# Kernel tuning notes

Hardware: AMD Instinct MI355X
Metric: run time of the kernel (lower is better)

## Reference

```python
import jax, jax.numpy as jnp
import numpy as np

N, E, B = 20000, 320000, 64   # nodes, edges, graphs
H, L = 32, 3                  # hidden dim (dim_inner), message passes
HH = H * H
IDX = jnp.array([[0, 1, 2, 3, 4, 5],
                 [1, 6, 7, 8, 9, 10],
                 [2, 7, 11, 12, 13, 14],
                 [3, 8, 12, 15, 16, 17],
                 [4, 9, 13, 16, 18, 19],
                 [5, 10, 14, 17, 19, 20]])


def setup_inputs() -> dict:
    key = jax.random.key(0)
    ks = iter(jax.random.split(key, 40))
    def nrm(shape, s=0.1):
        return jax.random.normal(next(ks), shape, jnp.float32) * s
    inp = {}
    inp['node_attrs'] = jax.random.normal(next(ks), (N, 1), jnp.float32)
    inp['positions'] = jax.random.normal(next(ks), (N, 3), jnp.float32)
    inp['shifts'] = jax.random.normal(next(ks), (E, 3), jnp.float32) * 0.01
    inp['edge_attr'] = jax.random.uniform(next(ks), (E, 1), jnp.float32)
    inp['edge_index'] = jax.random.randint(next(ks), (2, E), 0, N)
    inp['batch_ids'] = jax.random.randint(next(ks), (N,), 0, B)
    # node embedding Linear(1, H)
    inp['embed_W'] = nrm((1, H), 1.0)
    inp['embed_b'] = nrm((H,))
    # per-layer edge MLP: 5 -> H -> H -> H*H (all with bias), plus NNConv bias
    inp['e_W1'] = nrm((L, 5, H), 0.4)
    inp['e_b1'] = nrm((L, H))
    inp['e_W2'] = nrm((L, H, H), 0.15)
    inp['e_b2'] = nrm((L, H))
    inp['e_W3'] = nrm((L, H, HH), 0.15)
    inp['e_b3'] = nrm((L, HH))
    inp['conv_b'] = nrm((L, H))
    # head MLP: H -> 128 -> 64 -> 32 -> 21
    inp['h_W1'] = nrm((H, 128), 0.15)
    inp['h_b1'] = nrm((128,))
    inp['h_W2'] = nrm((128, 64), 0.1)
    inp['h_b2'] = nrm((64,))
    inp['h_W3'] = nrm((64, 32), 0.12)
    inp['h_b3'] = nrm((32,))
    inp['h_W4'] = nrm((32, 21), 0.18)
    inp['h_b4'] = nrm((21,))
    return inp


def reference(node_attrs, positions, shifts, edge_attr, edge_index, batch_ids,
              embed_W, embed_b, e_W1, e_b1, e_W2, e_b2, e_W3, e_b3, conv_b,
              h_W1, h_b1, h_W2, h_b2, h_W3, h_b3, h_W4, h_b4):
    src, dst = edge_index[0], edge_index[1]
    x = node_attrs @ embed_W + embed_b                       # [N, H]
    # get_edge_vectors_and_lengths (MACE convention): receiver - sender + shifts
    vec = positions[dst] - positions[src] + shifts            # [E, 3]
    length = jnp.linalg.norm(vec, axis=-1, keepdims=True)     # [E, 1]
    ef = jnp.concatenate([vec, length, edge_attr], axis=1)    # [E, 5]
    for i in range(L):
        h = jax.nn.relu(ef @ e_W1[i] + e_b1[i])
        h = jax.nn.relu(h @ e_W2[i] + e_b2[i])
        w = jax.nn.relu(h @ e_W3[i] + e_b3[i]).reshape(-1, H, H)  # [E, H, H]
        # NNConv message: x_j @ W_e, aggr='add', root_weight=False, bias=True
        msg = jnp.einsum('eh,ehk->ek', x[src], w)             # [E, H]
        agg = jax.ops.segment_sum(msg, dst, num_segments=N) + conv_b[i]
        x = x + jax.nn.relu(agg)
    # global mean pool over graphs
    ones = jnp.ones((x.shape[0], 1), x.dtype)
    counts = jax.ops.segment_sum(ones, batch_ids, num_segments=B)
    pooled = jax.ops.segment_sum(x, batch_ids, num_segments=B) / jnp.maximum(counts, 1.0)
    h = jax.nn.selu(pooled @ h_W1 + h_b1)
    h = jax.nn.selu(h @ h_W2 + h_b2)
    h = jax.nn.selu(h @ h_W3 + h_b3)
    out = h @ h_W4 + h_b4                                     # [B, 21]
    C = out[:, IDX]                                           # [B, 6, 6]
    return C
```

## Files before the change

### kernel.cpp

```cpp
#include <hip/hip_runtime.h>
#include <hip/hip_bf16.h>

#define N_ 20000
#define E_ 320000
#define B_ 64

typedef __attribute__((ext_vector_type(8))) short short8;
typedef __attribute__((ext_vector_type(4))) float f4;
typedef __attribute__((ext_vector_type(2))) float f2v;
typedef __attribute__((ext_vector_type(4))) unsigned int u4;
typedef __attribute__((ext_vector_type(4))) unsigned short us4;

union U8 { short s[8]; unsigned short us[8]; short8 v; u4 u; };
union F4 { f4 v; f2v h[2]; float f[4]; };

__device__ __forceinline__ float bs2f(unsigned short s) {
    return __uint_as_float(((unsigned int)s) << 16);
}
__device__ __forceinline__ unsigned short f2bs(float f) {
    unsigned int u = __float_as_uint(f);
    unsigned int r = u + 0x7FFFu + ((u >> 16) & 1u);
    return (unsigned short)(r >> 16);
}
__device__ __forceinline__ unsigned int pk2(float a, float b) {
    __hip_bfloat162 h = __float22bfloat162_rn(make_float2(a, b));
    union { __hip_bfloat162 h2; unsigned int u; } cv;
    cv.h2 = h;
    return cv.u;
}

#define WAVE_LDS_WAIT() asm volatile("s_waitcnt lgkmcnt(0)" ::: "memory")

#define MFMA_B16(a, b, c) __builtin_amdgcn_mfma_f32_16x16x32_bf16(a, b, c, 0, 0, 0)

__device__ __constant__ int c_IDX[36] = {
    0,1,2,3,4,5, 1,6,7,8,9,10, 2,7,11,12,13,14,
    3,8,12,15,16,17, 4,9,13,16,18,19, 5,10,14,17,19,20};

__global__ __launch_bounds__(256) void k_setup(
    const float* __restrict__ na, const float* __restrict__ eW, const float* __restrict__ eb,
    float* __restrict__ x, int* __restrict__ deg, int* __restrict__ bcnt,
    const float* __restrict__ pos, const float* __restrict__ shifts, const float* __restrict__ eattr,
    const int* __restrict__ eidx, unsigned short* __restrict__ efp,
    const float* __restrict__ w3, unsigned short* __restrict__ w3r,
    const float* __restrict__ w1, const float* __restrict__ w2,
    unsigned short* __restrict__ w1r, unsigned short* __restrict__ w2r,
    const int* __restrict__ batch) {
    int bid = blockIdx.x, t = threadIdx.x;
    if (bid < 625) {
        int tid = bid * 256 + t;
        int base = tid * 4;
        int n = tid >> 3, c = (tid & 7) * 4;
        float nv = na[n];
        F4 o;
        for (int r = 0; r < 4; ++r) o.f[r] = nv * eW[c + r] + eb[c + r];
        *(f4*)(x + base) = o.v;
    } else if (bid < 1875) {
        int e = (bid - 625) * 256 + t;
        int s = eidx[e], d = eidx[E_ + e];
        float vx = pos[d * 3 + 0] - pos[s * 3 + 0] + shifts[e * 3 + 0];
        float vy = pos[d * 3 + 1] - pos[s * 3 + 1] + shifts[e * 3 + 1];
        float vz = pos[d * 3 + 2] - pos[s * 3 + 2] + shifts[e * 3 + 2];
        float ln = sqrtf(vx * vx + vy * vy + vz * vz);
        u4 o;
        o[0] = pk2(vx, vy);
        o[1] = pk2(vz, ln);
        o[2] = pk2(eattr[e], 0.f);
        o[3] = 0u;
        *(u4*)(efp + (size_t)e * 8) = o;
        atomicAdd(&deg[d], 1);
    } else if (bid < 1923) {
        int tid = (bid - 1875) * 256 + t;
        int l = tid & 63, t2 = (tid >> 6) & 63, i = tid >> 12;
        int q = l >> 4, m = l & 15;
        U8 o;
        for (int j = 0; j < 8; ++j) {
            int k = q * 8 + j;
            o.us[j] = f2bs(w3[(i * 32 + k) * 1024 + t2 * 16 + m]);
        }
        *(u4*)(w3r + (size_t)tid * 8) = o.u;
    } else if (bid < 1926) {
        int tid = (bid - 1923) * 256 + t;
        bool isw2 = tid >= 384;
        int idx = isw2 ? tid - 384 : tid;
        int i = idx >> 7;
        int tau = (idx >> 6) & 1;
        int l = idx & 63;
        int q = l >> 4, m = l & 15;
        U8 o;
        for (int j = 0; j < 8; ++j) {
            int k = q * 8 + j;
            if (!isw2) o.us[j] = (k < 5) ? f2bs(w1[i * 160 + k * 32 + tau * 16 + m]) : (unsigned short)0;
            else       o.us[j] = f2bs(w2[i * 1024 + k * 32 + tau * 16 + m]);
        }
        unsigned short* dst = (isw2 ? w2r : w1r) + i * 1024 + tau * 512 + l * 8;
        *(u4*)dst = o.u;
    } else {
        __shared__ int s[64];
        if (t < 64) s[t] = 0;
        __syncthreads();
        int n = (bid - 1926) * 256 + t;
        if (n < N_) atomicAdd(&s[batch[n]], 1);
        __syncthreads();
        if (t < 64 && s[t]) atomicAdd(&bcnt[t], s[t]);
    }
}

__global__ __launch_bounds__(1024) void k_scans(const int* __restrict__ deg,
                                                int* __restrict__ off, int* __restrict__ cur,
                                                const int* __restrict__ bcnt,
                                                int* __restrict__ boff, int* __restrict__ bcur) {
    int t = threadIdx.x;
    if (blockIdx.x == 0) {
        __shared__ int shW[16];
        int base = t * 20;
        int loc[20]; int s = 0;
        for (int k = 0; k < 20; ++k) {
            int i = base + k;
            int v = (i < N_) ? deg[i] : 0;
            loc[k] = s; s += v;
        }
        int lane = t & 63, wv = t >> 6;
        int v = s;
        for (int d = 1; d < 64; d <<= 1) {
            int u = __shfl_up(v, d);
            if (lane >= d) v += u;
        }
        if (lane == 63) shW[wv] = v;
        __syncthreads();
        if (wv == 0) {
            int w = (lane < 16) ? shW[lane] : 0;
            for (int d = 1; d < 16; d <<= 1) {
                int u = __shfl_up(w, d);
                if (lane >= d) w += u;
            }
            if (lane < 16) shW[lane] = w;
        }
        __syncthreads();
        int woff = (wv > 0) ? shW[wv - 1] : 0;
        int incl = v + woff;
        int excl = incl - s;
        for (int k = 0; k < 20; ++k) {
            int i = base + k;
            if (i < N_) { int o = excl + loc[k]; off[i] = o; cur[i] = o; }
        }
        if (t == 1023) off[N_] = incl;
    } else {
        if (t < 64) {
            int v0 = bcnt[t];
            int v = v0;
            for (int d = 1; d < 64; d <<= 1) {
                int u = __shfl_up(v, d);
                if (t >= d) v += u;
            }
            boff[t] = v - v0; bcur[t] = v - v0;
            if (t == 63) boff[64] = v;
        }
    }
}

__global__ __launch_bounds__(256) void k_fills(const int* __restrict__ eidx,
                                               int* __restrict__ cur, int* __restrict__ rank,
                                               const int* __restrict__ batch,
                                               int* __restrict__ bcur, int* __restrict__ bperm) {
    int bid = blockIdx.x, t = threadIdx.x;
    if (bid < 1250) {
        int e = bid * 256 + t;
        rank[e] = atomicAdd(&cur[eidx[E_ + e]], 1);
    } else {
        int n = (bid - 1250) * 256 + t;
        if (n < N_) {
            int p = atomicAdd(&bcur[batch[n]], 1);
            bperm[p] = n;
        }
    }
}

template <bool STORE>
__global__ __launch_bounds__(256, 8) void k_edge(
    const unsigned short* __restrict__ efp, const int* __restrict__ eidx,
    const int* __restrict__ rank,
    const float* __restrict__ x, float* __restrict__ agg, unsigned short* __restrict__ msg,
    const unsigned short* __restrict__ w1r, const float* __restrict__ b1,
    const unsigned short* __restrict__ w2r, const float* __restrict__ b2,
    const unsigned short* __restrict__ w3r, const float* __restrict__ b3) {
    __shared__ float s_b3[1024];
    __shared__ __align__(16) unsigned short s_h[4][640];
    __shared__ __align__(16) unsigned short s_x[4][2][640];

    const int t = threadIdx.x;
    for (int k = t; k < 1024; k += 256) s_b3[k] = b3[k];

    const int wave = t >> 6, lane = t & 63;
    const int q = lane >> 4, e = lane & 15;
    const int ebase = (blockIdx.x * 4 + wave) * 32;

    for (int g = 0; g < 2; ++g) {
        int srce = eidx[ebase + g * 16 + e];
        const float* xp = x + srce * 32 + q * 8;
        F4 xa, xb2;
        xa.v = *(const f4*)xp;
        xb2.v = *(const f4*)(xp + 4);
        u4 P;
        P[0] = pk2(xa.f[0], xa.f[1]);
        P[1] = pk2(xa.f[2], xa.f[3]);
        P[2] = pk2(xb2.f[0], xb2.f[1]);
        P[3] = pk2(xb2.f[2], xb2.f[3]);
        *(u4*)&s_x[wave][g][e * 40 + q * 8] = P;
    }

    U8 w1f[2], w2f[2];
    float b1v[2][4], b2v[2][4];
    for (int tau = 0; tau < 2; ++tau) {
        w1f[tau].u = *(const u4*)(w1r + tau * 512 + lane * 8);
        w2f[tau].u = *(const u4*)(w2r + tau * 512 + lane * 8);
        for (int r = 0; r < 4; ++r) {
            b1v[tau][r] = b1[tau * 16 + q * 4 + r];
            b2v[tau][r] = b2[tau * 16 + q * 4 + r];
        }
    }

    const f4 z4 = {0.f, 0.f, 0.f, 0.f};
    short8 h2f[2];

    for (int g = 0; g < 2; ++g) {
        U8 ef;
        if (q == 0) ef.u = *(const u4*)(efp + (size_t)(ebase + g * 16 + e) * 8);
        else { u4 zz = {0u, 0u, 0u, 0u}; ef.u = zz; }

        f4 c0 = MFMA_B16(w1f[0].v, ef.v, z4);
        f4 c1 = MFMA_B16(w1f[1].v, ef.v, z4);
        uint2 pkw;
        pkw.x = pk2(fmaxf(c0[0] + b1v[0][0], 0.f), fmaxf(c0[1] + b1v[0][1], 0.f));
        pkw.y = pk2(fmaxf(c0[2] + b1v[0][2], 0.f), fmaxf(c0[3] + b1v[0][3], 0.f));
        *(uint2*)&s_h[wave][e * 40 + q * 4] = pkw;
        pkw.x = pk2(fmaxf(c1[0] + b1v[1][0], 0.f), fmaxf(c1[1] + b1v[1][1], 0.f));
        pkw.y = pk2(fmaxf(c1[2] + b1v[1][2], 0.f), fmaxf(c1[3] + b1v[1][3], 0.f));
        *(uint2*)&s_h[wave][e * 40 + 16 + q * 4] = pkw;
        WAVE_LDS_WAIT();
        short8 h1f = *(const short8*)&s_h[wave][e * 40 + q * 8];
        c0 = MFMA_B16(w2f[0].v, h1f, z4);
        c1 = MFMA_B16(w2f[1].v, h1f, z4);
        pkw.x = pk2(fmaxf(c0[0] + b2v[0][0], 0.f), fmaxf(c0[1] + b2v[0][1], 0.f));
        pkw.y = pk2(fmaxf(c0[2] + b2v[0][2], 0.f), fmaxf(c0[3] + b2v[0][3], 0.f));
        *(uint2*)&s_h[wave][e * 40 + q * 4] = pkw;
        pkw.x = pk2(fmaxf(c1[0] + b2v[1][0], 0.f), fmaxf(c1[1] + b2v[1][1], 0.f));
        pkw.y = pk2(fmaxf(c1[2] + b2v[1][2], 0.f), fmaxf(c1[3] + b2v[1][3], 0.f));
        *(uint2*)&s_h[wave][e * 40 + 16 + q * 4] = pkw;
        WAVE_LDS_WAIT();
        h2f[g] = *(const short8*)&s_h[wave][e * 40 + q * 8];
        WAVE_LDS_WAIT();
    }

    __syncthreads();

    F4 macc[2][2];
    macc[0][0].v = z4; macc[0][1].v = z4; macc[1][0].v = z4; macc[1][1].v = z4;

#pragma unroll 4
    for (int h = 0; h < 32; ++h) {
        short8 a0 = *(const short8*)(w3r + h * 1024 + lane * 8);
        short8 a1 = *(const short8*)(w3r + h * 1024 + 512 + lane * 8);
        f4 ci0 = *(const f4*)&s_b3[h * 32 + q * 4];
        f4 ci1 = *(const f4*)&s_b3[h * 32 + 16 + q * 4];
        for (int g = 0; g < 2; ++g) {
            float xv = bs2f(s_x[wave][g][e * 40 + h]);
            F4 d0, d1, m0, m1;
            d0.v = MFMA_B16(a0, h2f[g], ci0);
            d1.v = MFMA_B16(a1, h2f[g], ci1);
            for (int r = 0; r < 4; ++r) {
                m0.f[r] = fmaxf(d0.f[r], 0.f);
                m1.f[r] = fmaxf(d1.f[r], 0.f);
            }
            f2v xv2 = {xv, xv};
            macc[g][0].h[0] = __builtin_elementwise_fma(m0.h[0], xv2, macc[g][0].h[0]);
            macc[g][0].h[1] = __builtin_elementwise_fma(m0.h[1], xv2, macc[g][0].h[1]);
            macc[g][1].h[0] = __builtin_elementwise_fma(m1.h[0], xv2, macc[g][1].h[0]);
            macc[g][1].h[1] = __builtin_elementwise_fma(m1.h[1], xv2, macc[g][1].h[1]);
        }
    }

    if (STORE) {
        for (int g = 0; g < 2; ++g) {
            int rk = rank[ebase + g * 16 + e];
            unsigned short* mp = msg + (size_t)rk * 32 + q * 4;
            for (int p = 0; p < 2; ++p) {
                uint2 m;
                m.x = pk2(macc[g][p].f[0], macc[g][p].f[1]);
                m.y = pk2(macc[g][p].f[2], macc[g][p].f[3]);
                *(uint2*)(mp + p * 16) = m;
            }
        }
    } else {
        for (int g = 0; g < 2; ++g) {
            int dste = eidx[E_ + ebase + g * 16 + e];
            float* ap = agg + dste * 32 + q * 4;
            for (int p = 0; p < 2; ++p)
                for (int r = 0; r < 4; ++r)
                    atomicAdd(ap + p * 16 + r, macc[g][p].f[r]);
        }
    }
}

__global__ __launch_bounds__(256) void k_gather(const unsigned short* __restrict__ msg,
                                                const int* __restrict__ off,
                                                const float* __restrict__ cb,
                                                float* __restrict__ x) {
    int wave = threadIdx.x >> 6, lane = threadIdx.x & 63;
    int n = blockIdx.x * 4 + wave;
    if (n >= N_) return;
    int j0 = off[n], j1 = off[n + 1];
    const unsigned short* base = msg + (size_t)j0 * 32;
    int nchunk = (j1 - j0) * 4;
    float a[8] = {0.f, 0.f, 0.f, 0.f, 0.f, 0.f, 0.f, 0.f};
    for (int it = lane; it < nchunk; it += 64) {
        u4 v = *(const u4*)(base + it * 8);
        for (int m = 0; m < 4; ++m) {
            unsigned int w = v[m];
            a[2 * m]     += __uint_as_float(w << 16);
            a[2 * m + 1] += __uint_as_float(w & 0xffff0000u);
        }
    }
    for (int d = 4; d < 64; d <<= 1)
        for (int m = 0; m < 8; ++m)
            a[m] += __shfl_xor(a[m], d);
    if (lane < 4) {
        int c0 = lane * 8;
        float* xp = x + n * 32 + c0;
        F4 xa, xb2;
        xa.v = *(const f4*)xp;
        xb2.v = *(const f4*)(xp + 4);
        for (int i = 0; i < 4; ++i) {
            xa.f[i]  += fmaxf(a[i] + cb[c0 + i], 0.f);
            xb2.f[i] += fmaxf(a[4 + i] + cb[c0 + 4 + i], 0.f);
        }
        *(f4*)xp = xa.v;
        *(f4*)(xp + 4) = xb2.v;
    }
}

__device__ __forceinline__ float selu_(float v) {
    return 1.0507009873554805f * (v > 0.f ? v : 1.6732632423543772f * (expf(v) - 1.f));
}

__global__ __launch_bounds__(1024) void k_pool_head(const float* __restrict__ x,
                                                    const int* __restrict__ boff,
                                                    const int* __restrict__ bperm,
                                                    const float* __restrict__ W1, const float* __restrict__ b1,
                                                    const float* __restrict__ W2, const float* __restrict__ b2,
                                                    const float* __restrict__ W3, const float* __restrict__ b3,
                                                    const float* __restrict__ W4, const float* __restrict__ b4,
                                                    float* __restrict__ out) {
    __shared__ float sp[32][32];
    __shared__ float s0[32], s1[128], s2[64], s3[32], s4[21];
    int b = blockIdx.x, t = threadIdx.x, c = t & 31, slot = t >> 5;
    int j0 = boff[b], j1 = boff[b + 1];
    float a = 0.f;
    for (int j = j0 + slot; j < j1; j += 32)
        a += x[bperm[j] * 32 + c];
    sp[slot][c] = a;
    __syncthreads();
    if (t < 32) {
        float s = 0.f;
        for (int k = 0; k < 32; ++k) s += sp[k][t];
        s0[t] = s / fmaxf((float)(j1 - j0), 1.f);
    }
    __syncthreads();
    if (t < 128) {
        float v = b1[t];
        for (int cc = 0; cc < 32; ++cc) v += s0[cc] * W1[cc * 128 + t];
        s1[t] = selu_(v);
    }
    __syncthreads();
    if (t < 64) {
        float v = b2[t];
        for (int cc = 0; cc < 128; ++cc) v += s1[cc] * W2[cc * 64 + t];
        s2[t] = selu_(v);
    }
    __syncthreads();
    if (t < 32) {
        float v = b3[t];
        for (int cc = 0; cc < 64; ++cc) v += s2[cc] * W3[cc * 32 + t];
        s3[t] = selu_(v);
    }
    __syncthreads();
    if (t < 21) {
        float v = b4[t];
        for (int cc = 0; cc < 32; ++cc) v += s3[cc] * W4[cc * 21 + t];
        s4[t] = v;
    }
    __syncthreads();
    if (t < 36) out[b * 36 + t] = s4[c_IDX[t]];
}

__global__ __launch_bounds__(256) void k_init_fb(const float* __restrict__ na,
                                                 const float* __restrict__ eW,
                                                 const float* __restrict__ eb,
                                                 float* __restrict__ x, float* __restrict__ agg) {
    int tid = blockIdx.x * 256 + threadIdx.x;
    int n = tid >> 5, c = tid & 31;
    x[tid] = na[n] * eW[c] + eb[c];
    agg[tid] = 0.f;
}

__global__ __launch_bounds__(256) void k_prep_fb(const float* __restrict__ pos,
                                                 const float* __restrict__ shifts,
                                                 const float* __restrict__ eattr,
                                                 const int* __restrict__ eidx,
                                                 unsigned short* __restrict__ efp) {
    int e = blockIdx.x * 256 + threadIdx.x;
    int s = eidx[e], d = eidx[E_ + e];
    float vx = pos[d * 3 + 0] - pos[s * 3 + 0] + shifts[e * 3 + 0];
    float vy = pos[d * 3 + 1] - pos[s * 3 + 1] + shifts[e * 3 + 1];
    float vz = pos[d * 3 + 2] - pos[s * 3 + 2] + shifts[e * 3 + 2];
    float ln = sqrtf(vx * vx + vy * vy + vz * vz);
    u4 o;
    o[0] = pk2(vx, vy);
    o[1] = pk2(vz, ln);
    o[2] = pk2(eattr[e], 0.f);
    o[3] = 0u;
    *(u4*)(efp + (size_t)e * 8) = o;
}

__global__ __launch_bounds__(256) void k_repack_fb(const float* __restrict__ w3,
                                                   unsigned short* __restrict__ w3r,
                                                   const float* __restrict__ w1,
                                                   const float* __restrict__ w2,
                                                   unsigned short* __restrict__ w1r,
                                                   unsigned short* __restrict__ w2r) {
    int tid = blockIdx.x * 256 + threadIdx.x;
    if (tid < 12288) {
        int l = tid & 63, t2 = (tid >> 6) & 63, i = tid >> 12;
        int q = l >> 4, m = l & 15;
        U8 o;
        for (int j = 0; j < 8; ++j) {
            int k = q * 8 + j;
            o.us[j] = f2bs(w3[(i * 32 + k) * 1024 + t2 * 16 + m]);
        }
        *(u4*)(w3r + (size_t)tid * 8) = o.u;
    } else if (tid < 13056) {
        int t2 = tid - 12288;
        bool isw2 = t2 >= 384;
        int idx = isw2 ? t2 - 384 : t2;
        int i = idx >> 7, tau = (idx >> 6) & 1, l = idx & 63;
        int q = l >> 4, m = l & 15;
        U8 o;
        for (int j = 0; j < 8; ++j) {
            int k = q * 8 + j;
            if (!isw2) o.us[j] = (k < 5) ? f2bs(w1[i * 160 + k * 32 + tau * 16 + m]) : (unsigned short)0;
            else       o.us[j] = f2bs(w2[i * 1024 + k * 32 + tau * 16 + m]);
        }
        unsigned short* dst = (isw2 ? w2r : w1r) + i * 1024 + tau * 512 + l * 8;
        *(u4*)dst = o.u;
    }
}

__global__ __launch_bounds__(256) void k_node(float* __restrict__ x, float* __restrict__ agg,
                                              const float* __restrict__ cb) {
    int tid = blockIdx.x * 256 + threadIdx.x;
    int c = tid & 31;
    float a = agg[tid] + cb[c];
    x[tid] += fmaxf(a, 0.f);
    agg[tid] = 0.f;
}

__global__ __launch_bounds__(256) void k_zero_pool(float* __restrict__ pooled, int* __restrict__ cnt) {
    int tid = blockIdx.x * 256 + threadIdx.x;
    if (tid < 2048) pooled[tid] = 0.f;
    else if (tid < 2112) cnt[tid - 2048] = 0;
}

__global__ __launch_bounds__(256) void k_pool(const float* __restrict__ x, const int* __restrict__ batch,
                                              float* __restrict__ pooled, int* __restrict__ cnt) {
    int tid = blockIdx.x * 256 + threadIdx.x;
    int n = tid >> 5, c = tid & 31;
    int b = batch[n];
    atomicAdd(&pooled[b * 32 + c], x[tid]);
    if (c == 0) atomicAdd(&cnt[b], 1);
}

__global__ __launch_bounds__(128) void k_head(const float* __restrict__ pooled, const int* __restrict__ cnt,
                                              const float* __restrict__ W1, const float* __restrict__ b1,
                                              const float* __restrict__ W2, const float* __restrict__ b2,
                                              const float* __restrict__ W3, const float* __restrict__ b3,
                                              const float* __restrict__ W4, const float* __restrict__ b4,
                                              float* __restrict__ out) {
    __shared__ float s0[32], s1[128], s2[64], s3[32], s4[21];
    int b = blockIdx.x, t = threadIdx.x;
    if (t < 32) s0[t] = pooled[b * 32 + t] / fmaxf((float)cnt[b], 1.f);
    __syncthreads();
    {
        float a = b1[t];
        for (int c = 0; c < 32; ++c) a += s0[c] * W1[c * 128 + t];
        s1[t] = selu_(a);
    }
    __syncthreads();
    if (t < 64) {
        float a = b2[t];
        for (int c = 0; c < 128; ++c) a += s1[c] * W2[c * 64 + t];
        s2[t] = selu_(a);
    }
    __syncthreads();
    if (t < 32) {
        float a = b3[t];
        for (int c = 0; c < 64; ++c) a += s2[c] * W3[c * 32 + t];
        s3[t] = selu_(a);
    }
    __syncthreads();
    if (t < 21) {
        float a = b4[t];
        for (int c = 0; c < 32; ++c) a += s3[c] * W4[c * 21 + t];
        s4[t] = a;
    }
    __syncthreads();
    if (t < 36) out[b * 36 + t] = s4[c_IDX[t]];
}

extern "C" void kernel_launch(void* const* d_in, const int* in_sizes, int n_in,
                              void* d_out, int out_size, void* d_ws, size_t ws_size,
                              hipStream_t stream) {
    const float* na     = (const float*)d_in[0];
    const float* pos    = (const float*)d_in[1];
    const float* shifts = (const float*)d_in[2];
    const float* eattr  = (const float*)d_in[3];
    const int*   eidx   = (const int*)d_in[4];
    const int*   batch  = (const int*)d_in[5];
    const float* embW   = (const float*)d_in[6];
    const float* embB   = (const float*)d_in[7];
    const float* eW1    = (const float*)d_in[8];
    const float* eb1    = (const float*)d_in[9];
    const float* eW2    = (const float*)d_in[10];
    const float* eb2    = (const float*)d_in[11];
    const float* eW3    = (const float*)d_in[12];
    const float* eb3    = (const float*)d_in[13];
    const float* cvb    = (const float*)d_in[14];
    const float* hW1    = (const float*)d_in[15];
    const float* hb1    = (const float*)d_in[16];
    const float* hW2    = (const float*)d_in[17];
    const float* hb2    = (const float*)d_in[18];
    const float* hW3    = (const float*)d_in[19];
    const float* hb3    = (const float*)d_in[20];
    const float* hW4    = (const float*)d_in[21];
    const float* hb4    = (const float*)d_in[22];

    const size_t need_csr = (size_t)640000 * 4
                          + (size_t)(20000 + 64 + 20004 + 20000 + 320000 + 68 + 64 + 20000) * 4
                          + ((size_t)E_ * 8 + 98304 + 3072 + 3072 + (size_t)E_ * 32) * 2;

    if (ws_size >= need_csr) {
        char* ws = (char*)d_ws;
        float* x      = (float*)ws;
        int*   deg    = (int*)(x + 640000);
        int*   bcnt   = deg + 20000;
        int*   off    = bcnt + 64;
        int*   cur    = off + 20004;
        int*   rank   = cur + 20000;
        int*   boff   = rank + 320000;
        int*   bcur   = boff + 68;
        int*   bperm  = bcur + 64;
        unsigned short* efp = (unsigned short*)(bperm + 20000);
        unsigned short* w3r = efp + (size_t)E_ * 8;
        unsigned short* w1r = w3r + 98304;
        unsigned short* w2r = w1r + 3072;
        unsigned short* msg = w2r + 3072;

        hipMemsetAsync(deg, 0, (20000 + 64) * sizeof(int), stream);
        k_setup<<<2005, 256, 0, stream>>>(na, embW, embB, x, deg, bcnt,
                                          pos, shifts, eattr, eidx, efp,
                                          eW3, w3r, eW1, eW2, w1r, w2r, batch);
        k_scans<<<2, 1024, 0, stream>>>(deg, off, cur, bcnt, boff, bcur);
        k_fills<<<1329, 256, 0, stream>>>(eidx, cur, rank, batch, bcur, bperm);

        for (int i = 0; i < 3; ++i) {
            k_edge<true><<<2500, 256, 0, stream>>>(efp, eidx, rank, x, nullptr, msg,
                                                   w1r + i * 1024, eb1 + i * 32,
                                                   w2r + i * 1024, eb2 + i * 32,
                                                   w3r + i * 32768, eb3 + i * 1024);
            k_gather<<<5000, 256, 0, stream>>>(msg, off, cvb + i * 32, x);
        }

        k_pool_head<<<64, 1024, 0, stream>>>(x, boff, bperm,
                                             hW1, hb1, hW2, hb2, hW3, hb3, hW4, hb4,
                                             (float*)d_out);
    } else {
        char* ws = (char*)d_ws;
        float* x      = (float*)ws;
        float* agg    = x + 640000;
        float* pooled = agg + 640000;
        int*   cnt    = (int*)(pooled + 2048);
        unsigned short* efp = (unsigned short*)(cnt + 64);
        unsigned short* w3r = efp + (size_t)E_ * 8;
        unsigned short* w1r = w3r + 98304;
        unsigned short* w2r = w1r + 3072;

        k_init_fb<<<2500, 256, 0, stream>>>(na, embW, embB, x, agg);
        k_prep_fb<<<1250, 256, 0, stream>>>(pos, shifts, eattr, eidx, efp);
        k_repack_fb<<<51, 256, 0, stream>>>(eW3, w3r, eW1, eW2, w1r, w2r);
        k_zero_pool<<<9, 256, 0, stream>>>(pooled, cnt);

        for (int i = 0; i < 3; ++i) {
            k_edge<false><<<2500, 256, 0, stream>>>(efp, eidx, nullptr, x, agg, nullptr,
                                                    w1r + i * 1024, eb1 + i * 32,
                                                    w2r + i * 1024, eb2 + i * 32,
                                                    w3r + i * 32768, eb3 + i * 1024);
            k_node<<<2500, 256, 0, stream>>>(x, agg, cvb + i * 32);
        }

        k_pool<<<2500, 256, 0, stream>>>(x, batch, pooled, cnt);
        k_head<<<64, 128, 0, stream>>>(pooled, cnt, hW1, hb1, hW2, hb2, hW3, hb3, hW4, hb4,
                                       (float*)d_out);
    }
}
```

Before: 377.8 us.

## Write edge messages contiguously and gather via CSR permutation; vectorize ReLU

The edge kernel now writes each message at its own edge index instead of scattering to a rank-sorted slot. The gather kernel reads messages through a dst-sorted permutation array built in k_fills. This trades scattered 64-byte stores for indirect loads plus an extra perm read in the gather. It also raises the unroll of the W3 loop from 4 to 8 and uses packed float2 max for the ReLU, which may increase register pressure.

```diff
diff --git a/kernel.cpp b/kernel.cpp
--- a/kernel.cpp
+++ b/kernel.cpp
@@ -160,13 +160,14 @@
 }
 
 __global__ __launch_bounds__(256) void k_fills(const int* __restrict__ eidx,
-                                               int* __restrict__ cur, int* __restrict__ rank,
+                                               int* __restrict__ cur, int* __restrict__ perm,
                                                const int* __restrict__ batch,
                                                int* __restrict__ bcur, int* __restrict__ bperm) {
     int bid = blockIdx.x, t = threadIdx.x;
     if (bid < 1250) {
         int e = bid * 256 + t;
-        rank[e] = atomicAdd(&cur[eidx[E_ + e]], 1);
+        int p = atomicAdd(&cur[eidx[E_ + e]], 1);
+        perm[p] = e;
     } else {
         int n = (bid - 1250) * 256 + t;
         if (n < N_) {
@@ -179,7 +180,6 @@
 template <bool STORE>
 __global__ __launch_bounds__(256, 8) void k_edge(
     const unsigned short* __restrict__ efp, const int* __restrict__ eidx,
-    const int* __restrict__ rank,
     const float* __restrict__ x, float* __restrict__ agg, unsigned short* __restrict__ msg,
     const unsigned short* __restrict__ w1r, const float* __restrict__ b1,
     const unsigned short* __restrict__ w2r, const float* __restrict__ b2,
@@ -221,6 +221,7 @@
     }
 
     const f4 z4 = {0.f, 0.f, 0.f, 0.f};
+    const f2v z2 = {0.f, 0.f};
     short8 h2f[2];
 
     for (int g = 0; g < 2; ++g) {
@@ -257,7 +258,7 @@
     F4 macc[2][2];
     macc[0][0].v = z4; macc[0][1].v = z4; macc[1][0].v = z4; macc[1][1].v = z4;
 
-#pragma unroll 4
+#pragma unroll 8
     for (int h = 0; h < 32; ++h) {
         short8 a0 = *(const short8*)(w3r + h * 1024 + lane * 8);
         short8 a1 = *(const short8*)(w3r + h * 1024 + 512 + lane * 8);
@@ -268,10 +269,10 @@
             F4 d0, d1, m0, m1;
             d0.v = MFMA_B16(a0, h2f[g], ci0);
             d1.v = MFMA_B16(a1, h2f[g], ci1);
-            for (int r = 0; r < 4; ++r) {
-                m0.f[r] = fmaxf(d0.f[r], 0.f);
-                m1.f[r] = fmaxf(d1.f[r], 0.f);
-            }
+            m0.h[0] = __builtin_elementwise_max(d0.h[0], z2);
+            m0.h[1] = __builtin_elementwise_max(d0.h[1], z2);
+            m1.h[0] = __builtin_elementwise_max(d1.h[0], z2);
+            m1.h[1] = __builtin_elementwise_max(d1.h[1], z2);
             f2v xv2 = {xv, xv};
             macc[g][0].h[0] = __builtin_elementwise_fma(m0.h[0], xv2, macc[g][0].h[0]);
             macc[g][0].h[1] = __builtin_elementwise_fma(m0.h[1], xv2, macc[g][0].h[1]);
@@ -282,8 +283,7 @@
 
     if (STORE) {
         for (int g = 0; g < 2; ++g) {
-            int rk = rank[ebase + g * 16 + e];
-            unsigned short* mp = msg + (size_t)rk * 32 + q * 4;
+            unsigned short* mp = msg + (size_t)(ebase + g * 16 + e) * 32 + q * 4;
             for (int p = 0; p < 2; ++p) {
                 uint2 m;
                 m.x = pk2(macc[g][p].f[0], macc[g][p].f[1]);
@@ -304,17 +304,18 @@
 
 __global__ __launch_bounds__(256) void k_gather(const unsigned short* __restrict__ msg,
                                                 const int* __restrict__ off,
+                                                const int* __restrict__ perm,
                                                 const float* __restrict__ cb,
                                                 float* __restrict__ x) {
     int wave = threadIdx.x >> 6, lane = threadIdx.x & 63;
     int n = blockIdx.x * 4 + wave;
     if (n >= N_) return;
     int j0 = off[n], j1 = off[n + 1];
-    const unsigned short* base = msg + (size_t)j0 * 32;
     int nchunk = (j1 - j0) * 4;
     float a[8] = {0.f, 0.f, 0.f, 0.f, 0.f, 0.f, 0.f, 0.f};
     for (int it = lane; it < nchunk; it += 64) {
-        u4 v = *(const u4*)(base + it * 8);
+        int e2 = perm[j0 + (it >> 2)];
+        u4 v = *(const u4*)(msg + (size_t)e2 * 32 + (it & 3) * 8);
         for (int m = 0; m < 4; ++m) {
             unsigned int w = v[m];
             a[2 * m]     += __uint_as_float(w << 16);
@@ -554,8 +555,8 @@
         int*   bcnt   = deg + 20000;
         int*   off    = bcnt + 64;
         int*   cur    = off + 20004;
-        int*   rank   = cur + 20000;
-        int*   boff   = rank + 320000;
+        int*   perm   = cur + 20000;
+        int*   boff   = perm + 320000;
         int*   bcur   = boff + 68;
         int*   bperm  = bcur + 64;
         unsigned short* efp = (unsigned short*)(bperm + 20000);
@@ -569,14 +570,14 @@
                                           pos, shifts, eattr, eidx, efp,
                                           eW3, w3r, eW1, eW2, w1r, w2r, batch);
         k_scans<<<2, 1024, 0, stream>>>(deg, off, cur, bcnt, boff, bcur);
-        k_fills<<<1329, 256, 0, stream>>>(eidx, cur, rank, batch, bcur, bperm);
+        k_fills<<<1329, 256, 0, stream>>>(eidx, cur, perm, batch, bcur, bperm);
 
         for (int i = 0; i < 3; ++i) {
-            k_edge<true><<<2500, 256, 0, stream>>>(efp, eidx, rank, x, nullptr, msg,
+            k_edge<true><<<2500, 256, 0, stream>>>(efp, eidx, x, nullptr, msg,
                                                    w1r + i * 1024, eb1 + i * 32,
                                                    w2r + i * 1024, eb2 + i * 32,
                                                    w3r + i * 32768, eb3 + i * 1024);
-            k_gather<<<5000, 256, 0, stream>>>(msg, off, cvb + i * 32, x);
+            k_gather<<<5000, 256, 0, stream>>>(msg, off, perm, cvb + i * 32, x);
         }
 
         k_pool_head<<<64, 1024, 0, stream>>>(x, boff, bperm,
@@ -599,7 +600,7 @@
         k_zero_pool<<<9, 256, 0, stream>>>(pooled, cnt);
 
         for (int i = 0; i < 3; ++i) {
-            k_edge<false><<<2500, 256, 0, stream>>>(efp, eidx, nullptr, x, agg, nullptr,
+            k_edge<false><<<2500, 256, 0, stream>>>(efp, eidx, x, agg, nullptr,
                                                     w1r + i * 1024, eb1 + i * 32,
                                                     w2r + i * 1024, eb2 + i * 32,
                                                     w3r + i * 32768, eb3 + i * 1024);
```

New measurement: 573.8 us. 51.9% more time.
